# Kernel optimization log

Hardware: AMD Instinct MI355X
Metric: run time of the kernel (lower is better)

Reference implementation:

```python
import jax, jax.numpy as jnp
import numpy as np

FACTOR = 1.0

def _dct_matrix():
    n = 8
    D = np.zeros((n * n, n * n), dtype=np.float32)
    for u in range(n):
        for v in range(n):
            au = 1.0 / np.sqrt(2.0) if u == 0 else 1.0
            av = 1.0 / np.sqrt(2.0) if v == 0 else 1.0
            alpha = au * av * 0.25
            for x in range(n):
                for y in range(n):
                    D[u * n + v, x * n + y] = alpha * np.cos((2 * x + 1) * u * np.pi / 16) * np.cos((2 * y + 1) * v * np.pi / 16)
    return D

def _y_quant_table():
    t = np.array([[16, 11, 10, 16, 24, 40, 51, 61], [12, 12, 14, 19, 26, 58, 60, 55],
                  [14, 13, 16, 24, 40, 57, 69, 56], [14, 17, 22, 29, 51, 87, 80, 62],
                  [18, 22, 37, 56, 68, 109, 103, 77], [24, 35, 55, 64, 81, 104, 113, 92],
                  [49, 64, 78, 87, 103, 121, 120, 101], [72, 92, 95, 98, 112, 100, 103, 99]],
                 dtype=np.float32).T
    return t

def _c_quant_table():
    t = np.full((8, 8), 99, dtype=np.float32)
    t[:4, :4] = np.array([[17, 18, 24, 47], [18, 21, 26, 66], [24, 26, 56, 99], [47, 66, 99, 99]],
                          dtype=np.float32).T
    return t

_D = jnp.asarray(_dct_matrix())          # [64,64]
_QT = jnp.stack([jnp.asarray(_y_quant_table()),
                 jnp.asarray(_c_quant_table()),
                 jnp.asarray(_c_quant_table())], axis=0) * FACTOR  # [3,8,8]

def setup_inputs() -> dict:
    key = jax.random.key(0)
    image = jax.random.uniform(key, (32, 3, 512, 512), dtype=jnp.float32)
    return {"image": image}

def _diffjpeg(image):
    x = jnp.clip(image, 0.0, 1.0)
    B, C, H, W = x.shape  # H, W multiples of 8 -> no padding branch
    r, g, b = x[:, 0], x[:, 1], x[:, 2]
    y = 0.299 * r + 0.587 * g + 0.114 * b
    cb = (b - y) * 0.564 + 0.5
    cr = (r - y) * 0.713 + 0.5
    ycbcr = jnp.stack([y, cb, cr], axis=1)  # [B,3,H,W]
    # blockify into 8x8 tiles
    nh, nw = H // 8, W // 8
    blocks = ycbcr.reshape(B, C, nh, 8, nw, 8).transpose(0, 1, 2, 4, 3, 5)  # [B,C,nh,nw,8,8]
    flat = blocks.reshape(-1, 64) * 255.0 - 128.0
    dct = flat @ _D.T                      # matmul(D, flat.T).T
    dctb = dct.reshape(B, C, nh, nw, 8, 8)
    qte = _QT[None, :, None, None, :, :]   # [1,3,1,1,8,8]
    q = dctb / qte
    q = q + jax.lax.stop_gradient(jnp.round(q) - q)  # STE rounding
    deq = q * qte
    idct = deq.reshape(-1, 64) @ _D        # matmul(D.T, x.T).T
    idct = (idct + 128.0) / 255.0
    img = idct.reshape(B, C, nh, nw, 8, 8).transpose(0, 1, 2, 4, 3, 5).reshape(B, C, H, W)
    yy, ycb, ycr = img[:, 0], img[:, 1] - 0.5, img[:, 2] - 0.5
    rr = yy + 1.403 * ycr
    gg = yy - 0.714 * ycr - 0.344 * ycb
    bb = yy + 1.773 * ycb
    rgb = jnp.clip(jnp.stack([rr, gg, bb], axis=1), 0.0, 1.0)
    return jnp.clip(rgb, 0.0, 1.0)

def reference(image):
    return _diffjpeg(image)
```

## Files before the change

kernel.cpp:

```cpp
#include <hip/hip_runtime.h>

typedef float f32x2 __attribute__((ext_vector_type(2)));

#define K4 0.353553391f
#define K1 0.490392640f
#define K3 0.415734806f
#define K5 0.277785117f
#define K7 0.097545161f
#define K2 0.461939766f
#define K6 0.191341716f

__device__ __align__(16) const float YQT[64] = {
    16.f, 12.f, 14.f, 14.f,  18.f,  24.f,  49.f,  72.f,
    11.f, 12.f, 13.f, 17.f,  22.f,  35.f,  64.f,  92.f,
    10.f, 14.f, 16.f, 22.f,  37.f,  55.f,  78.f,  95.f,
    16.f, 19.f, 24.f, 29.f,  56.f,  64.f,  87.f,  98.f,
    24.f, 26.f, 40.f, 51.f,  68.f,  81.f, 103.f, 112.f,
    40.f, 58.f, 57.f, 87.f, 109.f, 104.f, 121.f, 100.f,
    51.f, 60.f, 69.f, 80.f, 103.f, 113.f, 120.f, 103.f,
    61.f, 55.f, 56.f, 62.f,  77.f,  92.f, 101.f,  99.f
};
__device__ __align__(16) const float RYQT[64] = {
    1.f/16.f, 1.f/12.f, 1.f/14.f, 1.f/14.f, 1.f/18.f,  1.f/24.f,  1.f/49.f,  1.f/72.f,
    1.f/11.f, 1.f/12.f, 1.f/13.f, 1.f/17.f, 1.f/22.f,  1.f/35.f,  1.f/64.f,  1.f/92.f,
    1.f/10.f, 1.f/14.f, 1.f/16.f, 1.f/22.f, 1.f/37.f,  1.f/55.f,  1.f/78.f,  1.f/95.f,
    1.f/16.f, 1.f/19.f, 1.f/24.f, 1.f/29.f, 1.f/56.f,  1.f/64.f,  1.f/87.f,  1.f/98.f,
    1.f/24.f, 1.f/26.f, 1.f/40.f, 1.f/51.f, 1.f/68.f,  1.f/81.f,  1.f/103.f, 1.f/112.f,
    1.f/40.f, 1.f/58.f, 1.f/57.f, 1.f/87.f, 1.f/109.f, 1.f/104.f, 1.f/121.f, 1.f/100.f,
    1.f/51.f, 1.f/60.f, 1.f/69.f, 1.f/80.f, 1.f/103.f, 1.f/113.f, 1.f/120.f, 1.f/103.f,
    1.f/61.f, 1.f/55.f, 1.f/56.f, 1.f/62.f, 1.f/77.f,  1.f/92.f,  1.f/101.f, 1.f/99.f
};
__device__ __align__(16) const float CQ[64] = {
    17.f, 18.f, 24.f, 47.f, 99.f, 99.f, 99.f, 99.f,
    18.f, 21.f, 26.f, 66.f, 99.f, 99.f, 99.f, 99.f,
    24.f, 26.f, 56.f, 99.f, 99.f, 99.f, 99.f, 99.f,
    47.f, 66.f, 99.f, 99.f, 99.f, 99.f, 99.f, 99.f,
    99.f, 99.f, 99.f, 99.f, 99.f, 99.f, 99.f, 99.f,
    99.f, 99.f, 99.f, 99.f, 99.f, 99.f, 99.f, 99.f,
    99.f, 99.f, 99.f, 99.f, 99.f, 99.f, 99.f, 99.f,
    99.f, 99.f, 99.f, 99.f, 99.f, 99.f, 99.f, 99.f
};
__device__ __align__(16) const float RCQ[64] = {
    1.f/17.f, 1.f/18.f, 1.f/24.f, 1.f/47.f, 1.f/99.f, 1.f/99.f, 1.f/99.f, 1.f/99.f,
    1.f/18.f, 1.f/21.f, 1.f/26.f, 1.f/66.f, 1.f/99.f, 1.f/99.f, 1.f/99.f, 1.f/99.f,
    1.f/24.f, 1.f/26.f, 1.f/56.f, 1.f/99.f, 1.f/99.f, 1.f/99.f, 1.f/99.f, 1.f/99.f,
    1.f/47.f, 1.f/66.f, 1.f/99.f, 1.f/99.f, 1.f/99.f, 1.f/99.f, 1.f/99.f, 1.f/99.f,
    1.f/99.f, 1.f/99.f, 1.f/99.f, 1.f/99.f, 1.f/99.f, 1.f/99.f, 1.f/99.f, 1.f/99.f,
    1.f/99.f, 1.f/99.f, 1.f/99.f, 1.f/99.f, 1.f/99.f, 1.f/99.f, 1.f/99.f, 1.f/99.f,
    1.f/99.f, 1.f/99.f, 1.f/99.f, 1.f/99.f, 1.f/99.f, 1.f/99.f, 1.f/99.f, 1.f/99.f,
    1.f/99.f, 1.f/99.f, 1.f/99.f, 1.f/99.f, 1.f/99.f, 1.f/99.f, 1.f/99.f, 1.f/99.f
};

__device__ __forceinline__ float gfma(float a, float b, float c) { return fmaf(a, b, c); }
__device__ __forceinline__ f32x2 gfma(f32x2 a, f32x2 b, f32x2 c) { return __builtin_elementwise_fma(a, b, c); }
__device__ __forceinline__ f32x2 gfma(float a, f32x2 b, f32x2 c) { return __builtin_elementwise_fma((f32x2){a, a}, b, c); }

template <typename T>
__device__ __forceinline__ void dct8(const T x[8], T X[8]) {
    const T a0 = x[0] + x[7], a1 = x[1] + x[6], a2 = x[2] + x[5], a3 = x[3] + x[4];
    const T d0 = x[0] - x[7], d1 = x[1] - x[6], d2 = x[2] - x[5], d3 = x[3] - x[4];
    const T e0 = a0 + a3, e1 = a1 + a2, f0 = a0 - a3, f1 = a1 - a2;
    X[0] = K4 * (e0 + e1);
    X[4] = K4 * (e0 - e1);
    X[2] = gfma(K6, f1, K2 * f0);
    X[6] = gfma(-K2, f1, K6 * f0);
    X[1] = gfma(K7, d3, gfma(K5, d2, gfma(K3, d1, K1 * d0)));
    X[3] = gfma(-K5, d3, gfma(-K1, d2, gfma(-K7, d1, K3 * d0)));
    X[5] = gfma(K3, d3, gfma(K7, d2, gfma(-K1, d1, K5 * d0)));
    X[7] = gfma(-K1, d3, gfma(K3, d2, gfma(-K5, d1, K7 * d0)));
}

template <typename T>
__device__ __forceinline__ void idct8(const T X[8], T x[8]) {
    const T g0 = K4 * (X[0] + X[4]);
    const T g1 = K4 * (X[0] - X[4]);
    const T E0 = gfma(K6, X[6], gfma(K2, X[2], g0));
    const T E1 = gfma(-K2, X[6], gfma(K6, X[2], g1));
    const T E2 = gfma(K2, X[6], gfma(-K6, X[2], g1));
    const T E3 = gfma(-K6, X[6], gfma(-K2, X[2], g0));
    const T O0 = gfma(K7, X[7], gfma(K5, X[5], gfma(K3, X[3], K1 * X[1])));
    const T O1 = gfma(-K5, X[7], gfma(-K1, X[5], gfma(-K7, X[3], K3 * X[1])));
    const T O2 = gfma(K3, X[7], gfma(K7, X[5], gfma(-K1, X[3], K5 * X[1])));
    const T O3 = gfma(-K1, X[7], gfma(K3, X[5], gfma(-K5, X[3], K7 * X[1])));
    x[0] = E0 + O0;  x[7] = E0 - O0;
    x[1] = E1 + O1;  x[6] = E1 - O1;
    x[2] = E2 + O2;  x[5] = E2 - O2;
    x[3] = E3 + O3;  x[4] = E3 - O3;
}

__device__ __forceinline__ f32x2 quant2(f32x2 sv, f32x2 qt, f32x2 rq) {
    const f32x2 q0 = sv * rq;
    const f32x2 e  = gfma(-qt, q0, sv);
    const f32x2 q  = gfma(rq, e, q0);
    const f32x2 n  = {rintf(q.x), rintf(q.y)};
    return n * qt;
}

__device__ __forceinline__ void wave_lds_fence() {
    asm volatile("s_waitcnt lgkmcnt(0)" ::: "memory");
}

#define LDSW 68

__global__ __launch_bounds__(256, 6) void diffjpeg_kernel(const float* __restrict__ in,
                                                          float* __restrict__ out)
{
    __shared__ __align__(16) float pl[3][32][LDSW];

    const int t  = threadIdx.x;
    const int l  = t & 63;
    const int wv = t >> 6;
    const int r0 = wv * 8;

    const int bid  = blockIdx.x;
    const int img  = bid >> 7;
    const int rem  = bid & 127;
    const int trow = rem >> 3;
    const int tcol = rem & 7;
    const size_t HW = (size_t)512 * 512;
    const size_t sbase = (size_t)img * 3 * HW + (size_t)(trow * 32 + wv * 8) * 512 + (size_t)(tcol * 64);
    const float* __restrict__ pin  = in  + sbase;
    float* __restrict__       pout = out + sbase;

    {
        const float* cb = pin + l;
        float rv[8], gv[8], bv[8];
        #pragma unroll
        for (int x = 0; x < 8; ++x) rv[x] = cb[(size_t)x * 512];
        #pragma unroll
        for (int x = 0; x < 8; ++x) gv[x] = cb[HW + (size_t)x * 512];
        #pragma unroll
        for (int x = 0; x < 8; ++x) bv[x] = cb[2 * HW + (size_t)x * 512];

        float yv[8];
        f32x2 cc[8];
        #pragma unroll
        for (int x = 0; x < 8; ++x) {
            const float r = fminf(fmaxf(rv[x], 0.f), 1.f);
            const float g = fminf(fmaxf(gv[x], 0.f), 1.f);
            const float b = fminf(fmaxf(bv[x], 0.f), 1.f);
            const float Y = fmaf(76.245f, r, fmaf(149.685f, g, 29.07f * b));
            yv[x] = Y - 128.f;
            const f32x2 tbr = gfma(255.f, (f32x2){b, r}, (f32x2){-Y, -Y});
            cc[x] = gfma((f32x2){0.564f, 0.713f}, tbr, (f32x2){-0.5f, -0.5f});
        }

        float X0[8];
        f32x2 XC[8];
        dct8(yv, X0);
        dct8(cc, XC);
        #pragma unroll
        for (int u = 0; u < 8; ++u) {
            pl[0][r0 + u][l] = X0[u];
            pl[1][r0 + u][l] = XC[u].x;
            pl[2][r0 + u][l] = XC[u].y;
        }
    }
    wave_lds_fence();

    {
        const int b8 = (l >> 3) * 8;
        const int rr = l & 7;

        const float4* yq4  = (const float4*)&YQT[rr * 8];
        const float4* ryq4 = (const float4*)&RYQT[rr * 8];
        const float4* cq4  = (const float4*)&CQ[rr * 8];
        const float4* rcq4 = (const float4*)&RCQ[rr * 8];
        const float4 yqa = yq4[0],  yqb = yq4[1];
        const float4 rya = ryq4[0], ryb = ryq4[1];
        const float4 cqa = cq4[0],  cqb = cq4[1];
        const float4 rca = rcq4[0], rcb4 = rcq4[1];
        const float yq[8]  = {yqa.x, yqa.y, yqa.z, yqa.w, yqb.x, yqb.y, yqb.z, yqb.w};
        const float ryq[8] = {rya.x, rya.y, rya.z, rya.w, ryb.x, ryb.y, ryb.z, ryb.w};
        const float cq[8]  = {cqa.x, cqa.y, cqa.z, cqa.w, cqb.x, cqb.y, cqb.z, cqb.w};
        const float rcq[8] = {rca.x, rca.y, rca.z, rca.w, rcb4.x, rcb4.y, rcb4.z, rcb4.w};

        {
            float4* rp = (float4*)&pl[0][r0 + rr][b8];
            const float4 a0 = rp[0];
            const float4 a1 = rp[1];
            const float T[8] = {a0.x, a0.y, a0.z, a0.w, a1.x, a1.y, a1.z, a1.w};
            float S[8];
            dct8(T, S);
            float Dq[8];
            #pragma unroll
            for (int i = 0; i < 4; ++i) {
                const f32x2 d = quant2((f32x2){S[2*i], S[2*i+1]},
                                       (f32x2){yq[2*i], yq[2*i+1]},
                                       (f32x2){ryq[2*i], ryq[2*i+1]});
                Dq[2*i] = d.x; Dq[2*i+1] = d.y;
            }
            float o[8];
            idct8(Dq, o);
            rp[0] = make_float4(o[0], o[1], o[2], o[3]);
            rp[1] = make_float4(o[4], o[5], o[6], o[7]);
        }

        {
            float4* rpb = (float4*)&pl[1][r0 + rr][b8];
            float4* rpr = (float4*)&pl[2][r0 + rr][b8];
            const float4 c0 = rpb[0], c1 = rpb[1];
            const float4 e0 = rpr[0], e1 = rpr[1];
            const f32x2 T[8] = {{c0.x, e0.x}, {c0.y, e0.y}, {c0.z, e0.z}, {c0.w, e0.w},
                                {c1.x, e1.x}, {c1.y, e1.y}, {c1.z, e1.z}, {c1.w, e1.w}};
            f32x2 S[8];
            dct8(T, S);
            f32x2 Dq[8];
            #pragma unroll
            for (int v = 0; v < 8; ++v)
                Dq[v] = quant2(S[v], (f32x2){cq[v], cq[v]}, (f32x2){rcq[v], rcq[v]});
            f32x2 o[8];
            idct8(Dq, o);
            rpb[0] = make_float4(o[0].x, o[1].x, o[2].x, o[3].x);
            rpb[1] = make_float4(o[4].x, o[5].x, o[6].x, o[7].x);
            rpr[0] = make_float4(o[0].y, o[1].y, o[2].y, o[3].y);
            rpr[1] = make_float4(o[4].y, o[5].y, o[6].y, o[7].y);
        }
    }
    wave_lds_fence();

    {
        float Xy[8];
        f32x2 Xc[8];
        #pragma unroll
        for (int u = 0; u < 8; ++u) {
            Xy[u] = pl[0][r0 + u][l];
            Xc[u] = (f32x2){pl[1][r0 + u][l], pl[2][r0 + u][l]};
        }
        float sy[8];
        f32x2 sc[8];
        idct8(Xy, sy);
        idct8(Xc, sc);

        float* ob = pout + l;
        constexpr float inv255 = 1.0f / 255.0f;
        constexpr float Kr = 0.504711754f;
        constexpr float Kg = 0.499886280f;
        constexpr float Kb = 0.505437240f;
        #pragma unroll
        for (int x = 0; x < 8; ++x) {
            const float scb = sc[x].x;
            const float scr = sc[x].y;
            const f32x2 inner = gfma((f32x2){1.403f, 1.773f}, (f32x2){scr, scb},
                                     (f32x2){sy[x], sy[x]});
            const f32x2 rb = gfma(inv255, inner, (f32x2){Kr, Kb});
            const float gg = fmaf(inv255, fmaf(-0.714f, scr, fmaf(-0.344f, scb, sy[x])), Kg);
            __builtin_nontemporal_store(fminf(fmaxf(rb.x, 0.f), 1.f), ob + (size_t)x * 512);
            __builtin_nontemporal_store(fminf(fmaxf(gg,   0.f), 1.f), ob + HW + (size_t)x * 512);
            __builtin_nontemporal_store(fminf(fmaxf(rb.y, 0.f), 1.f), ob + 2 * HW + (size_t)x * 512);
        }
    }
}

extern "C" void kernel_launch(void* const* d_in, const int* in_sizes, int n_in,
                              void* d_out, int out_size, void* d_ws, size_t ws_size,
                              hipStream_t stream) {
    const float* in = (const float*)d_in[0];
    float* out = (float*)d_out;
    const int B = in_sizes[0] / (3 * 512 * 512);
    const int grid = B * 128;
    diffjpeg_kernel<<<grid, 256, 0, stream>>>(in, out);
}
```

Before: 35.50 us.

## Process four tile rows per block with register prefetch of next tile

Each block now loops over four 32-row tiles in a 128-row band, and the grid shrinks by four. The next tile's RGB values are loaded into registers while the current tile's DCT, quantisation and IDCT run, so global loads overlap with compute. Launch bounds drop to 4 blocks per CU to leave room for the extra prefetch registers, and the clamps use fmed3. The trade-off is fewer resident waves and fewer blocks, which reduces parallelism for latency hiding on a memory-bound kernel.

```diff
diff --git a/kernel.cpp b/kernel.cpp
--- a/kernel.cpp
+++ b/kernel.cpp
@@ -54,6 +54,8 @@
 __device__ __forceinline__ float gfma(float a, float b, float c) { return fmaf(a, b, c); }
 __device__ __forceinline__ f32x2 gfma(f32x2 a, f32x2 b, f32x2 c) { return __builtin_elementwise_fma(a, b, c); }
 __device__ __forceinline__ f32x2 gfma(float a, f32x2 b, f32x2 c) { return __builtin_elementwise_fma((f32x2){a, a}, b, c); }
+
+__device__ __forceinline__ float clamp01(float x) { return __builtin_amdgcn_fmed3f(x, 0.f, 1.f); }
 
 template <typename T>
 __device__ __forceinline__ void dct8(const T x[8], T X[8]) {
@@ -102,7 +104,7 @@
 
 #define LDSW 68
 
-__global__ __launch_bounds__(256, 6) void diffjpeg_kernel(const float* __restrict__ in,
+__global__ __launch_bounds__(256, 4) void diffjpeg_kernel(const float* __restrict__ in,
                                                           float* __restrict__ out)
 {
     __shared__ __align__(16) float pl[3][32][LDSW];
@@ -113,141 +115,153 @@
     const int r0 = wv * 8;
 
     const int bid  = blockIdx.x;
-    const int img  = bid >> 7;
-    const int rem  = bid & 127;
-    const int trow = rem >> 3;
+    const int img  = bid >> 5;
+    const int rem  = bid & 31;
+    const int band = rem >> 3;
     const int tcol = rem & 7;
     const size_t HW = (size_t)512 * 512;
-    const size_t sbase = (size_t)img * 3 * HW + (size_t)(trow * 32 + wv * 8) * 512 + (size_t)(tcol * 64);
-    const float* __restrict__ pin  = in  + sbase;
-    float* __restrict__       pout = out + sbase;
-
-    {
-        const float* cb = pin + l;
-        float rv[8], gv[8], bv[8];
-        #pragma unroll
-        for (int x = 0; x < 8; ++x) rv[x] = cb[(size_t)x * 512];
-        #pragma unroll
-        for (int x = 0; x < 8; ++x) gv[x] = cb[HW + (size_t)x * 512];
-        #pragma unroll
-        for (int x = 0; x < 8; ++x) bv[x] = cb[2 * HW + (size_t)x * 512];
-
+    const size_t sbase = (size_t)img * 3 * HW + (size_t)(band * 128 + wv * 8) * 512 + (size_t)(tcol * 64);
+    const float* __restrict__ pin  = in  + sbase + l;
+    float* __restrict__       pout = out + sbase + l;
+    const size_t istep = (size_t)32 * 512;
+
+    float rv[8], gv[8], bv[8];
+    #pragma unroll
+    for (int x = 0; x < 8; ++x) rv[x] = pin[(size_t)x * 512];
+    #pragma unroll
+    for (int x = 0; x < 8; ++x) gv[x] = pin[HW + (size_t)x * 512];
+    #pragma unroll
+    for (int x = 0; x < 8; ++x) bv[x] = pin[2 * HW + (size_t)x * 512];
+
+    for (int it = 0; it < 4; ++it) {
         float yv[8];
         f32x2 cc[8];
         #pragma unroll
         for (int x = 0; x < 8; ++x) {
-            const float r = fminf(fmaxf(rv[x], 0.f), 1.f);
-            const float g = fminf(fmaxf(gv[x], 0.f), 1.f);
-            const float b = fminf(fmaxf(bv[x], 0.f), 1.f);
+            const float r = clamp01(rv[x]);
+            const float g = clamp01(gv[x]);
+            const float b = clamp01(bv[x]);
             const float Y = fmaf(76.245f, r, fmaf(149.685f, g, 29.07f * b));
             yv[x] = Y - 128.f;
             const f32x2 tbr = gfma(255.f, (f32x2){b, r}, (f32x2){-Y, -Y});
             cc[x] = gfma((f32x2){0.564f, 0.713f}, tbr, (f32x2){-0.5f, -0.5f});
         }
 
-        float X0[8];
-        f32x2 XC[8];
-        dct8(yv, X0);
-        dct8(cc, XC);
-        #pragma unroll
-        for (int u = 0; u < 8; ++u) {
-            pl[0][r0 + u][l] = X0[u];
-            pl[1][r0 + u][l] = XC[u].x;
-            pl[2][r0 + u][l] = XC[u].y;
-        }
-    }
-    wave_lds_fence();
-
-    {
-        const int b8 = (l >> 3) * 8;
-        const int rr = l & 7;
-
-        const float4* yq4  = (const float4*)&YQT[rr * 8];
-        const float4* ryq4 = (const float4*)&RYQT[rr * 8];
-        const float4* cq4  = (const float4*)&CQ[rr * 8];
-        const float4* rcq4 = (const float4*)&RCQ[rr * 8];
-        const float4 yqa = yq4[0],  yqb = yq4[1];
-        const float4 rya = ryq4[0], ryb = ryq4[1];
-        const float4 cqa = cq4[0],  cqb = cq4[1];
-        const float4 rca = rcq4[0], rcb4 = rcq4[1];
-        const float yq[8]  = {yqa.x, yqa.y, yqa.z, yqa.w, yqb.x, yqb.y, yqb.z, yqb.w};
-        const float ryq[8] = {rya.x, rya.y, rya.z, rya.w, ryb.x, ryb.y, ryb.z, ryb.w};
-        const float cq[8]  = {cqa.x, cqa.y, cqa.z, cqa.w, cqb.x, cqb.y, cqb.z, cqb.w};
-        const float rcq[8] = {rca.x, rca.y, rca.z, rca.w, rcb4.x, rcb4.y, rcb4.z, rcb4.w};
+        if (it < 3) {
+            const float* pn = pin + (size_t)(it + 1) * istep;
+            #pragma unroll
+            for (int x = 0; x < 8; ++x) rv[x] = pn[(size_t)x * 512];
+            #pragma unroll
+            for (int x = 0; x < 8; ++x) gv[x] = pn[HW + (size_t)x * 512];
+            #pragma unroll
+            for (int x = 0; x < 8; ++x) bv[x] = pn[2 * HW + (size_t)x * 512];
+        }
 
         {
-            float4* rp = (float4*)&pl[0][r0 + rr][b8];
-            const float4 a0 = rp[0];
-            const float4 a1 = rp[1];
-            const float T[8] = {a0.x, a0.y, a0.z, a0.w, a1.x, a1.y, a1.z, a1.w};
-            float S[8];
-            dct8(T, S);
-            float Dq[8];
-            #pragma unroll
-            for (int i = 0; i < 4; ++i) {
-                const f32x2 d = quant2((f32x2){S[2*i], S[2*i+1]},
-                                       (f32x2){yq[2*i], yq[2*i+1]},
-                                       (f32x2){ryq[2*i], ryq[2*i+1]});
-                Dq[2*i] = d.x; Dq[2*i+1] = d.y;
-            }
-            float o[8];
-            idct8(Dq, o);
-            rp[0] = make_float4(o[0], o[1], o[2], o[3]);
-            rp[1] = make_float4(o[4], o[5], o[6], o[7]);
-        }
+            float X0[8];
+            f32x2 XC[8];
+            dct8(yv, X0);
+            dct8(cc, XC);
+            #pragma unroll
+            for (int u = 0; u < 8; ++u) {
+                pl[0][r0 + u][l] = X0[u];
+                pl[1][r0 + u][l] = XC[u].x;
+                pl[2][r0 + u][l] = XC[u].y;
+            }
+        }
+        wave_lds_fence();
 
         {
-            float4* rpb = (float4*)&pl[1][r0 + rr][b8];
-            float4* rpr = (float4*)&pl[2][r0 + rr][b8];
-            const float4 c0 = rpb[0], c1 = rpb[1];
-            const float4 e0 = rpr[0], e1 = rpr[1];
-            const f32x2 T[8] = {{c0.x, e0.x}, {c0.y, e0.y}, {c0.z, e0.z}, {c0.w, e0.w},
-                                {c1.x, e1.x}, {c1.y, e1.y}, {c1.z, e1.z}, {c1.w, e1.w}};
-            f32x2 S[8];
-            dct8(T, S);
-            f32x2 Dq[8];
-            #pragma unroll
-            for (int v = 0; v < 8; ++v)
-                Dq[v] = quant2(S[v], (f32x2){cq[v], cq[v]}, (f32x2){rcq[v], rcq[v]});
-            f32x2 o[8];
-            idct8(Dq, o);
-            rpb[0] = make_float4(o[0].x, o[1].x, o[2].x, o[3].x);
-            rpb[1] = make_float4(o[4].x, o[5].x, o[6].x, o[7].x);
-            rpr[0] = make_float4(o[0].y, o[1].y, o[2].y, o[3].y);
-            rpr[1] = make_float4(o[4].y, o[5].y, o[6].y, o[7].y);
-        }
-    }
-    wave_lds_fence();
-
-    {
-        float Xy[8];
-        f32x2 Xc[8];
-        #pragma unroll
-        for (int u = 0; u < 8; ++u) {
-            Xy[u] = pl[0][r0 + u][l];
-            Xc[u] = (f32x2){pl[1][r0 + u][l], pl[2][r0 + u][l]};
-        }
-        float sy[8];
-        f32x2 sc[8];
-        idct8(Xy, sy);
-        idct8(Xc, sc);
-
-        float* ob = pout + l;
-        constexpr float inv255 = 1.0f / 255.0f;
-        constexpr float Kr = 0.504711754f;
-        constexpr float Kg = 0.499886280f;
-        constexpr float Kb = 0.505437240f;
-        #pragma unroll
-        for (int x = 0; x < 8; ++x) {
-            const float scb = sc[x].x;
-            const float scr = sc[x].y;
-            const f32x2 inner = gfma((f32x2){1.403f, 1.773f}, (f32x2){scr, scb},
-                                     (f32x2){sy[x], sy[x]});
-            const f32x2 rb = gfma(inv255, inner, (f32x2){Kr, Kb});
-            const float gg = fmaf(inv255, fmaf(-0.714f, scr, fmaf(-0.344f, scb, sy[x])), Kg);
-            __builtin_nontemporal_store(fminf(fmaxf(rb.x, 0.f), 1.f), ob + (size_t)x * 512);
-            __builtin_nontemporal_store(fminf(fmaxf(gg,   0.f), 1.f), ob + HW + (size_t)x * 512);
-            __builtin_nontemporal_store(fminf(fmaxf(rb.y, 0.f), 1.f), ob + 2 * HW + (size_t)x * 512);
+            const int b8 = (l >> 3) * 8;
+            const int rr = l & 7;
+
+            const float4* yq4  = (const float4*)&YQT[rr * 8];
+            const float4* ryq4 = (const float4*)&RYQT[rr * 8];
+            const float4* cq4  = (const float4*)&CQ[rr * 8];
+            const float4* rcq4 = (const float4*)&RCQ[rr * 8];
+            const float4 yqa = yq4[0],  yqb = yq4[1];
+            const float4 rya = ryq4[0], ryb = ryq4[1];
+            const float4 cqa = cq4[0],  cqb = cq4[1];
+            const float4 rca = rcq4[0], rcb4 = rcq4[1];
+            const float yq[8]  = {yqa.x, yqa.y, yqa.z, yqa.w, yqb.x, yqb.y, yqb.z, yqb.w};
+            const float ryq[8] = {rya.x, rya.y, rya.z, rya.w, ryb.x, ryb.y, ryb.z, ryb.w};
+            const float cq[8]  = {cqa.x, cqa.y, cqa.z, cqa.w, cqb.x, cqb.y, cqb.z, cqb.w};
+            const float rcq[8] = {rca.x, rca.y, rca.z, rca.w, rcb4.x, rcb4.y, rcb4.z, rcb4.w};
+
+            {
+                float4* rp = (float4*)&pl[0][r0 + rr][b8];
+                const float4 a0 = rp[0];
+                const float4 a1 = rp[1];
+                const float T[8] = {a0.x, a0.y, a0.z, a0.w, a1.x, a1.y, a1.z, a1.w};
+                float S[8];
+                dct8(T, S);
+                float Dq[8];
+                #pragma unroll
+                for (int i = 0; i < 4; ++i) {
+                    const f32x2 d = quant2((f32x2){S[2*i], S[2*i+1]},
+                                           (f32x2){yq[2*i], yq[2*i+1]},
+                                           (f32x2){ryq[2*i], ryq[2*i+1]});
+                    Dq[2*i] = d.x; Dq[2*i+1] = d.y;
+                }
+                float o[8];
+                idct8(Dq, o);
+                rp[0] = make_float4(o[0], o[1], o[2], o[3]);
+                rp[1] = make_float4(o[4], o[5], o[6], o[7]);
+            }
+
+            {
+                float4* rpb = (float4*)&pl[1][r0 + rr][b8];
+                float4* rpr = (float4*)&pl[2][r0 + rr][b8];
+                const float4 c0 = rpb[0], c1 = rpb[1];
+                const float4 e0 = rpr[0], e1 = rpr[1];
+                const f32x2 T[8] = {{c0.x, e0.x}, {c0.y, e0.y}, {c0.z, e0.z}, {c0.w, e0.w},
+                                    {c1.x, e1.x}, {c1.y, e1.y}, {c1.z, e1.z}, {c1.w, e1.w}};
+                f32x2 S[8];
+                dct8(T, S);
+                f32x2 Dq[8];
+                #pragma unroll
+                for (int v = 0; v < 8; ++v)
+                    Dq[v] = quant2(S[v], (f32x2){cq[v], cq[v]}, (f32x2){rcq[v], rcq[v]});
+                f32x2 o[8];
+                idct8(Dq, o);
+                rpb[0] = make_float4(o[0].x, o[1].x, o[2].x, o[3].x);
+                rpb[1] = make_float4(o[4].x, o[5].x, o[6].x, o[7].x);
+                rpr[0] = make_float4(o[0].y, o[1].y, o[2].y, o[3].y);
+                rpr[1] = make_float4(o[4].y, o[5].y, o[6].y, o[7].y);
+            }
+        }
+        wave_lds_fence();
+
+        {
+            float Xy[8];
+            f32x2 Xc[8];
+            #pragma unroll
+            for (int u = 0; u < 8; ++u) {
+                Xy[u] = pl[0][r0 + u][l];
+                Xc[u] = (f32x2){pl[1][r0 + u][l], pl[2][r0 + u][l]};
+            }
+            float sy[8];
+            f32x2 sc[8];
+            idct8(Xy, sy);
+            idct8(Xc, sc);
+
+            float* ob = pout + (size_t)it * istep;
+            constexpr float inv255 = 1.0f / 255.0f;
+            constexpr float Kr = 0.504711754f;
+            constexpr float Kg = 0.499886280f;
+            constexpr float Kb = 0.505437240f;
+            #pragma unroll
+            for (int x = 0; x < 8; ++x) {
+                const float scb = sc[x].x;
+                const float scr = sc[x].y;
+                const f32x2 inner = gfma((f32x2){1.403f, 1.773f}, (f32x2){scr, scb},
+                                         (f32x2){sy[x], sy[x]});
+                const f32x2 rb = gfma(inv255, inner, (f32x2){Kr, Kb});
+                const float gg = fmaf(inv255, fmaf(-0.714f, scr, fmaf(-0.344f, scb, sy[x])), Kg);
+                __builtin_nontemporal_store(clamp01(rb.x), ob + (size_t)x * 512);
+                __builtin_nontemporal_store(clamp01(gg),   ob + HW + (size_t)x * 512);
+                __builtin_nontemporal_store(clamp01(rb.y), ob + 2 * HW + (size_t)x * 512);
+            }
         }
     }
 }
@@ -258,6 +272,6 @@
     const float* in = (const float*)d_in[0];
     float* out = (float*)d_out;
     const int B = in_sizes[0] / (3 * 512 * 512);
-    const int grid = B * 128;
+    const int grid = B * 32;
     diffjpeg_kernel<<<grid, 256, 0, stream>>>(in, out);
 }
```

Result: no change. 36.08 us (+1.6%).
